# Performance work log

Measured on AMD Instinct MI355X. Metric: run time of the kernel, lower is better.

## Reference

```python
import jax, jax.numpy as jnp
import numpy as np

VOXEL_SIZE = 0.4
GAMMA = 1.1  # VoxelPointsSampler.GAMMA
GRID = 376   # (75.2 - (-75.2)) / 0.4


def setup_inputs() -> dict:
    key = jax.random.key(0)
    k1, k2, k3, k4, k5 = jax.random.split(key, 5)
    V, K, F, R, S = 20000, 16, 5, 256, 128
    pc_start = jnp.array([-75.2, -75.2], dtype=jnp.float32)
    coords = jax.random.randint(k1, (V, 2), 0, GRID, dtype=jnp.int32)  # voxel (x,y) grid coords
    centers = coords.astype(jnp.float32) * VOXEL_SIZE + pc_start
    voxels = jax.random.normal(k2, (V, K, F), dtype=jnp.float32)
    # place point xy near their voxel center so the radius search is non-trivial
    voxels = voxels.at[:, :, :2].multiply(0.2)
    voxels = voxels.at[:, :, :2].add(centers[:, None, :])
    num_points = jax.random.randint(k3, (V,), 0, K + 1, dtype=jnp.int32)
    bxy = jax.random.uniform(k4, (R, 2), jnp.float32, -70.0, 70.0)   # box centers x,y
    brest = jax.random.uniform(k5, (R, 5), jnp.float32)
    boxes = jnp.concatenate(
        [bxy, brest[:, :1], brest[:, 1:3] * 4.0 + 1.0, brest[:, 3:]], axis=1
    )  # [R,7]: x,y,z,dx,dy,dz,heading with dx,dy in [1,5]
    return {
        "voxels": voxels,
        "boxes": boxes,
        "pc_start": pc_start,
        "coords": coords,
        "num_points": num_points,
        "num_sample": S,
    }


def reference(voxels, boxes, pc_start, coords, num_points, num_sample):
    # voxels: [V,K,F] voxelized points; boxes: [R,7] ROIs; coords: [V,2] voxel (x,y) grid coords
    V, K, F = voxels.shape
    dt = voxels.dtype
    # --- voxel-level radius search (forward hot path) ---
    query_coords = (boxes[:, :2] - pc_start) / VOXEL_SIZE            # [R,2]
    radii_vox = jnp.linalg.norm(boxes[:, 3:5] * 0.5, axis=-1) * GAMMA / VOXEL_SIZE  # [R]
    dist = jnp.linalg.norm(query_coords[:, None, :] - coords[None, :, :].astype(dt), axis=-1)  # [R,V]
    voxel_mask = jnp.any(dist < radii_vox[:, None], axis=0)          # [V]
    # --- per-voxel valid-point mask (arange(k) < num_points), combined with voxel_mask ---
    pt_valid = (jnp.arange(K)[None, :] < num_points[:, None]) & voxel_mask[:, None]  # [V,K]
    pts = voxels.reshape(V * K, F)                                   # [N,F], N = V*K
    valid = pt_valid.reshape(V * K)                                  # [N]
    # --- cylindrical pool: per-ROI radius mask over points + topk sampling ---
    radii = jnp.linalg.norm(boxes[:, 3:5] * 0.5, axis=-1) * GAMMA    # [R]
    dis = jnp.linalg.norm(pts[None, :, :2] - boxes[:, None, :2], axis=-1)  # [R,N]
    point_mask = (dis <= radii[:, None]) & valid[None, :]            # [R,N]
    sampled_mask, sampled_idx = jax.lax.top_k(point_mask.astype(dt), num_sample)  # [R,S]
    key_points = jnp.take(pts, sampled_idx, axis=0) * sampled_mask[..., None]     # [R,S,F]
    return key_points, sampled_mask, voxel_mask
```

## Files before the change

kernel.cpp:

```cpp
#include <hip/hip_runtime.h>
#include <hip/hip_bf16.h>
#include <stdint.h>

#define VOXEL_SIZE_F 0.4f
#define GAMMA_F 1.1f
#define SLACK_F 0.0625f

__device__ __forceinline__ float sq2_rn(float dx, float dy) {
    return __fadd_rn(__fmul_rn(dx, dx), __fmul_rn(dy, dy));
}

__device__ __forceinline__ int wave_incl_scan(int v, int lane) {
    #pragma unroll
    for (int d = 1; d < 64; d <<= 1) {
        int t = __shfl_up(v, d, 64);
        if (lane >= d) v += t;
    }
    return v;
}

__global__ void k1_mask(const float* __restrict__ boxes,
                        const float* __restrict__ pc_start,
                        const int* __restrict__ coords,
                        const int* __restrict__ num_points,
                        const float* __restrict__ voxels,
                        int V, int R, int K, int F,
                        unsigned char* __restrict__ vstat,
                        float* __restrict__ vmaxoff,
                        float* __restrict__ out_vox,
                        int* __restrict__ bc) {
    __shared__ float qx[256], qy[256], rv[256];
    int lane = threadIdx.x;
    int v = blockIdx.x * 64 + lane;
    float psx = pc_start[0], psy = pc_start[1];
    float cxf = 0.f, cyf = 0.f;
    int np = 0;
    if (v < V) {
        cxf = (float)coords[2 * v];
        cyf = (float)coords[2 * v + 1];
        np = num_points[v];
        np = np < 0 ? 0 : (np > K ? K : np);
    }
    int m = 0;
    for (int rb = 0; rb < R; rb += 256) {
        int tile = (R - rb) < 256 ? (R - rb) : 256;
        for (int j = lane; j < tile; j += 64) {
            const float* bp = boxes + (size_t)(rb + j) * 7;
            float hx = bp[3] * 0.5f, hy = bp[4] * 0.5f;
            qx[j] = (bp[0] - psx) / VOXEL_SIZE_F;
            qy[j] = (bp[1] - psy) / VOXEL_SIZE_F;
            rv[j] = (sqrtf(sq2_rn(hx, hy)) * GAMMA_F) / VOXEL_SIZE_F;
        }
        __syncthreads();
        #pragma unroll 4
        for (int j = 0; j < tile; j++) {
            float dx = qx[j] - cxf, dy = qy[j] - cyf;
            m |= (sqrtf(sq2_rn(dx, dy)) < rv[j]) ? 1 : 0;
        }
        __syncthreads();
    }
    int am = (v < V) ? m : 0;
    unsigned long long bal = __ballot(am != 0);
    if (lane == 0) bc[blockIdx.x] = __popcll(bal);
    float mo = -1e30f;
    if (am && np > 0) {
        float cxm = cxf * VOXEL_SIZE_F + psx;
        float cym = cyf * VOXEL_SIZE_F + psy;
        const float* pv = voxels + (size_t)v * K * F;
        for (int k = 0; k < np; k++) {
            float px = pv[k * F + 0], py = pv[k * F + 1];
            float d = sqrtf(sq2_rn(px - cxm, py - cym));
            mo = fmaxf(mo, d);
        }
    }
    if (v < V) {
        vstat[v] = am ? (unsigned char)(np + 1) : 0;
        vmaxoff[v] = mo;
        out_vox[v] = am ? 1.0f : 0.0f;
    }
}

__global__ void k2_compact(const unsigned char* __restrict__ vstat,
                           const float* __restrict__ vmaxoff,
                           const int* __restrict__ coords,
                           const float* __restrict__ pc_start,
                           int V, int nb,
                           const int* __restrict__ bc,
                           float4* __restrict__ actq,
                           int* __restrict__ act_count) {
    __shared__ int sbase;
    int b = blockIdx.x;
    int lane = threadIdx.x;
    if (lane == 0) sbase = 0;
    __syncthreads();
    int run = 0;
    for (int i0 = 0; i0 < nb; i0 += 64) {
        int i = i0 + lane;
        int val = (i < nb) ? bc[i] : 0;
        int incl = wave_incl_scan(val, lane);
        if (i == b) sbase = run + incl - val;
        run += __shfl(incl, 63, 64);
    }
    if (b == 0 && lane == 0) *act_count = run;
    __syncthreads();
    int base = sbase;

    int v = b * 64 + lane;
    int stat = (v < V) ? (int)vstat[v] : 0;
    int m = stat > 0;
    unsigned long long bal = __ballot(m != 0);
    unsigned long long ltmask = (1ull << lane) - 1ull;
    int rank = __popcll(bal & ltmask);
    if (m) {
        float psx = pc_start[0], psy = pc_start[1];
        float cxm = (float)coords[2 * v] * VOXEL_SIZE_F + psx;
        float cym = (float)coords[2 * v + 1] * VOXEL_SIZE_F + psy;
        float4 q;
        q.x = cxm;
        q.y = cym;
        q.z = vmaxoff[v];
        q.w = __int_as_float(v | ((stat - 1) << 16));
        actq[base + rank] = q;
    }
}

__global__ void k3_roi(const float* __restrict__ voxels,
                       const float* __restrict__ boxes,
                       const float4* __restrict__ actq,
                       const int* __restrict__ act_count,
                       int K, int F, int S,
                       float* __restrict__ out_kp,
                       float* __restrict__ out_mask) {
    __shared__ float4 cq[256];
    __shared__ int wsum[4];
    int r = blockIdx.x;
    int tid = threadIdx.x, lane = tid & 63, wid = tid >> 6;
    unsigned long long ltmask = (1ull << lane) - 1ull;

    const float* bp = boxes + (size_t)r * 7;
    float bx = bp[0], by = bp[1];
    float hx = bp[3] * 0.5f, hy = bp[4] * 0.5f;
    float rad = sqrtf(sq2_rn(hx, hy)) * GAMMA_F;
    int A = *act_count;
    int count = 0;

    for (int c0 = 0; c0 < A && count < S; c0 += 256) {
        int i = c0 + tid;
        int pred = 0;
        float4 q = make_float4(0.f, 0.f, 0.f, 0.f);
        if (i < A) {
            q = actq[i];
            float d = sqrtf(sq2_rn(q.x - bx, q.y - by));
            pred = (d <= rad + q.z + SLACK_F) ? 1 : 0;
        }
        unsigned long long bal = __ballot(pred != 0);
        if (lane == 0) wsum[wid] = __popcll(bal);
        __syncthreads();
        int cb = 0;
        for (int w = 0; w < wid; w++) cb += wsum[w];
        int tot = wsum[0] + wsum[1] + wsum[2] + wsum[3];
        if (pred) cq[cb + __popcll(bal & ltmask)] = q;
        __syncthreads();

        for (int g0 = 0; g0 < tot && count < S; g0 += 16) {
            int ci = g0 + (tid >> 4), k = tid & 15;
            int pred2 = 0;
            size_t n = 0;
            if (ci < tot) {
                float4 qq = cq[ci];
                int vn = __float_as_int(qq.w);
                int npv = vn >> 16, vid = vn & 0xFFFF;
                if (k < npv) {
                    n = (size_t)(vid * K + k);
                    float px = voxels[n * F + 0], py = voxels[n * F + 1];
                    pred2 = (sqrtf(sq2_rn(px - bx, py - by)) <= rad) ? 1 : 0;
                }
            }
            unsigned long long bal2 = __ballot(pred2 != 0);
            if (lane == 0) wsum[wid] = __popcll(bal2);
            __syncthreads();
            int wb = count;
            for (int w = 0; w < wid; w++) wb += wsum[w];
            int tot2 = wsum[0] + wsum[1] + wsum[2] + wsum[3];
            int pos = wb + __popcll(bal2 & ltmask);
            if (pred2 && pos < S) {
                const float* src = voxels + n * F;
                float* dst = out_kp + ((size_t)r * S + pos) * F;
                #pragma unroll
                for (int j = 0; j < 5; j++) dst[j] = src[j];
            }
            count += tot2;
            __syncthreads();
        }
    }

    int sc = count < S ? count : S;
    for (int s = tid; s < S; s += 256)
        out_mask[(size_t)r * S + s] = (s < sc) ? 1.0f : 0.0f;
    for (int j = tid; j < S * F; j += 256) {
        int s = j / F;
        if (s >= sc) out_kp[(size_t)r * S * F + j] = 0.0f;
    }
}

extern "C" void kernel_launch(void* const* d_in, const int* in_sizes, int n_in,
                              void* d_out, int out_size, void* d_ws, size_t ws_size,
                              hipStream_t stream) {
    const float* voxels   = (const float*)d_in[0];
    const float* boxes    = (const float*)d_in[1];
    const float* pc_start = (const float*)d_in[2];
    const int*   coords   = (const int*)d_in[3];
    const int*   num_pts  = (const int*)d_in[4];

    int V = in_sizes[4];
    int R = in_sizes[1] / 7;
    int K = 16;
    int F = (in_sizes[0] / V) / K;
    int S = (out_size - V) / (R * (F + 1));
    int nb = (V + 63) / 64;

    float* out_kp  = (float*)d_out;
    float* out_msk = out_kp + (size_t)R * S * F;
    float* out_vox = out_msk + (size_t)R * S;

    char* w = (char*)d_ws;
    auto carve = [&](size_t bytes) {
        void* p = (void*)w;
        w += (bytes + 255) & ~(size_t)255;
        return p;
    };
    unsigned char* vstat   = (unsigned char*)carve((size_t)V);
    float*         vmaxoff = (float*)carve((size_t)V * 4);
    int*           bc      = (int*)carve((size_t)nb * 4);
    int*           actcnt  = (int*)carve(4);
    float4*        actq    = (float4*)carve((size_t)V * 16);

    k1_mask<<<nb, 64, 0, stream>>>(boxes, pc_start, coords, num_pts, voxels,
                                   V, R, K, F, vstat, vmaxoff, out_vox, bc);
    k2_compact<<<nb, 64, 0, stream>>>(vstat, vmaxoff, coords, pc_start,
                                      V, nb, bc, actq, actcnt);
    k3_roi<<<R, 256, 0, stream>>>(voxels, boxes, actq, actcnt,
                                  K, F, S, out_kp, out_msk);
}
```

Measured before the change: 111.5 us.

## Fuse mask, compaction and ROI sampling into one kernel with grid barrier

Replaces the three-kernel pipeline with a single persistent kernel. Each block first computes voxel masks and per-voxel records for 256 voxels, then waits at a software grid barrier (atomic counter) before doing per-ROI sampling. The separate compaction pass is dropped: ROI blocks scan all V records directly, and inactive voxels are skipped through a max-offset sentinel and a block-wide count early-out. This removes two kernel launches and the prefix-scan step, but each ROI now scans all voxels rather than only active ones. It also depends on all 256 blocks being co-resident for the spin barrier, and adds a memset launch.

```diff
diff --git a/kernel.cpp b/kernel.cpp
--- a/kernel.cpp
+++ b/kernel.cpp
@@ -10,196 +10,144 @@
     return __fadd_rn(__fmul_rn(dx, dx), __fmul_rn(dy, dy));
 }
 
-__device__ __forceinline__ int wave_incl_scan(int v, int lane) {
-    #pragma unroll
-    for (int d = 1; d < 64; d <<= 1) {
-        int t = __shfl_up(v, d, 64);
-        if (lane >= d) v += t;
-    }
-    return v;
-}
+__global__ __launch_bounds__(256) void k_fused(
+    const float* __restrict__ voxels,
+    const float* __restrict__ boxes,
+    const float* __restrict__ pc_start,
+    const int* __restrict__ coords,
+    const int* __restrict__ num_points,
+    int V, int R, int K, int F, int S,
+    float4* __restrict__ recq,
+    int* __restrict__ bar,
+    float* __restrict__ out_kp,
+    float* __restrict__ out_mask,
+    float* __restrict__ out_vox)
+{
+    __shared__ float qx[256], qy[256], rv[256];
+    __shared__ float4 cq[256];
+    __shared__ int wsum[4];
+    int tid = threadIdx.x, lane = tid & 63, wid = tid >> 6;
+    int b = blockIdx.x;
+    unsigned long long ltmask = (1ull << lane) - 1ull;
+    float psx = pc_start[0], psy = pc_start[1];
 
-__global__ void k1_mask(const float* __restrict__ boxes,
-                        const float* __restrict__ pc_start,
-                        const int* __restrict__ coords,
-                        const int* __restrict__ num_points,
-                        const float* __restrict__ voxels,
-                        int V, int R, int K, int F,
-                        unsigned char* __restrict__ vstat,
-                        float* __restrict__ vmaxoff,
-                        float* __restrict__ out_vox,
-                        int* __restrict__ bc) {
-    __shared__ float qx[256], qy[256], rv[256];
-    int lane = threadIdx.x;
-    int v = blockIdx.x * 64 + lane;
-    float psx = pc_start[0], psy = pc_start[1];
-    float cxf = 0.f, cyf = 0.f;
-    int np = 0;
-    if (v < V) {
-        cxf = (float)coords[2 * v];
-        cyf = (float)coords[2 * v + 1];
-        np = num_points[v];
-        np = np < 0 ? 0 : (np > K ? K : np);
-    }
-    int m = 0;
-    for (int rb = 0; rb < R; rb += 256) {
-        int tile = (R - rb) < 256 ? (R - rb) : 256;
-        for (int j = lane; j < tile; j += 64) {
-            const float* bp = boxes + (size_t)(rb + j) * 7;
+    int v = b * 256 + tid;
+    if (b * 256 < V) {
+        for (int j = tid; j < R; j += 256) {
+            const float* bp = boxes + (size_t)j * 7;
             float hx = bp[3] * 0.5f, hy = bp[4] * 0.5f;
             qx[j] = (bp[0] - psx) / VOXEL_SIZE_F;
             qy[j] = (bp[1] - psy) / VOXEL_SIZE_F;
             rv[j] = (sqrtf(sq2_rn(hx, hy)) * GAMMA_F) / VOXEL_SIZE_F;
         }
         __syncthreads();
-        #pragma unroll 4
-        for (int j = 0; j < tile; j++) {
-            float dx = qx[j] - cxf, dy = qy[j] - cyf;
-            m |= (sqrtf(sq2_rn(dx, dy)) < rv[j]) ? 1 : 0;
-        }
-        __syncthreads();
-    }
-    int am = (v < V) ? m : 0;
-    unsigned long long bal = __ballot(am != 0);
-    if (lane == 0) bc[blockIdx.x] = __popcll(bal);
-    float mo = -1e30f;
-    if (am && np > 0) {
-        float cxm = cxf * VOXEL_SIZE_F + psx;
-        float cym = cyf * VOXEL_SIZE_F + psy;
-        const float* pv = voxels + (size_t)v * K * F;
-        for (int k = 0; k < np; k++) {
-            float px = pv[k * F + 0], py = pv[k * F + 1];
-            float d = sqrtf(sq2_rn(px - cxm, py - cym));
-            mo = fmaxf(mo, d);
-        }
-    }
-    if (v < V) {
-        vstat[v] = am ? (unsigned char)(np + 1) : 0;
-        vmaxoff[v] = mo;
-        out_vox[v] = am ? 1.0f : 0.0f;
-    }
-}
-
-__global__ void k2_compact(const unsigned char* __restrict__ vstat,
-                           const float* __restrict__ vmaxoff,
-                           const int* __restrict__ coords,
-                           const float* __restrict__ pc_start,
-                           int V, int nb,
-                           const int* __restrict__ bc,
-                           float4* __restrict__ actq,
-                           int* __restrict__ act_count) {
-    __shared__ int sbase;
-    int b = blockIdx.x;
-    int lane = threadIdx.x;
-    if (lane == 0) sbase = 0;
-    __syncthreads();
-    int run = 0;
-    for (int i0 = 0; i0 < nb; i0 += 64) {
-        int i = i0 + lane;
-        int val = (i < nb) ? bc[i] : 0;
-        int incl = wave_incl_scan(val, lane);
-        if (i == b) sbase = run + incl - val;
-        run += __shfl(incl, 63, 64);
-    }
-    if (b == 0 && lane == 0) *act_count = run;
-    __syncthreads();
-    int base = sbase;
-
-    int v = b * 64 + lane;
-    int stat = (v < V) ? (int)vstat[v] : 0;
-    int m = stat > 0;
-    unsigned long long bal = __ballot(m != 0);
-    unsigned long long ltmask = (1ull << lane) - 1ull;
-    int rank = __popcll(bal & ltmask);
-    if (m) {
-        float psx = pc_start[0], psy = pc_start[1];
-        float cxm = (float)coords[2 * v] * VOXEL_SIZE_F + psx;
-        float cym = (float)coords[2 * v + 1] * VOXEL_SIZE_F + psy;
-        float4 q;
-        q.x = cxm;
-        q.y = cym;
-        q.z = vmaxoff[v];
-        q.w = __int_as_float(v | ((stat - 1) << 16));
-        actq[base + rank] = q;
-    }
-}
-
-__global__ void k3_roi(const float* __restrict__ voxels,
-                       const float* __restrict__ boxes,
-                       const float4* __restrict__ actq,
-                       const int* __restrict__ act_count,
-                       int K, int F, int S,
-                       float* __restrict__ out_kp,
-                       float* __restrict__ out_mask) {
-    __shared__ float4 cq[256];
-    __shared__ int wsum[4];
-    int r = blockIdx.x;
-    int tid = threadIdx.x, lane = tid & 63, wid = tid >> 6;
-    unsigned long long ltmask = (1ull << lane) - 1ull;
-
-    const float* bp = boxes + (size_t)r * 7;
-    float bx = bp[0], by = bp[1];
-    float hx = bp[3] * 0.5f, hy = bp[4] * 0.5f;
-    float rad = sqrtf(sq2_rn(hx, hy)) * GAMMA_F;
-    int A = *act_count;
-    int count = 0;
-
-    for (int c0 = 0; c0 < A && count < S; c0 += 256) {
-        int i = c0 + tid;
-        int pred = 0;
-        float4 q = make_float4(0.f, 0.f, 0.f, 0.f);
-        if (i < A) {
-            q = actq[i];
-            float d = sqrtf(sq2_rn(q.x - bx, q.y - by));
-            pred = (d <= rad + q.z + SLACK_F) ? 1 : 0;
-        }
-        unsigned long long bal = __ballot(pred != 0);
-        if (lane == 0) wsum[wid] = __popcll(bal);
-        __syncthreads();
-        int cb = 0;
-        for (int w = 0; w < wid; w++) cb += wsum[w];
-        int tot = wsum[0] + wsum[1] + wsum[2] + wsum[3];
-        if (pred) cq[cb + __popcll(bal & ltmask)] = q;
-        __syncthreads();
-
-        for (int g0 = 0; g0 < tot && count < S; g0 += 16) {
-            int ci = g0 + (tid >> 4), k = tid & 15;
-            int pred2 = 0;
-            size_t n = 0;
-            if (ci < tot) {
-                float4 qq = cq[ci];
-                int vn = __float_as_int(qq.w);
-                int npv = vn >> 16, vid = vn & 0xFFFF;
-                if (k < npv) {
-                    n = (size_t)(vid * K + k);
-                    float px = voxels[n * F + 0], py = voxels[n * F + 1];
-                    pred2 = (sqrtf(sq2_rn(px - bx, py - by)) <= rad) ? 1 : 0;
+        if (v < V) {
+            float cxf = (float)coords[2 * v], cyf = (float)coords[2 * v + 1];
+            int np = num_points[v];
+            np = np < 0 ? 0 : (np > K ? K : np);
+            int m = 0;
+            #pragma unroll 4
+            for (int j = 0; j < R; j++) {
+                float dx = qx[j] - cxf, dy = qy[j] - cyf;
+                m |= (sqrtf(sq2_rn(dx, dy)) < rv[j]) ? 1 : 0;
+            }
+            float cxm = cxf * VOXEL_SIZE_F + psx;
+            float cym = cyf * VOXEL_SIZE_F + psy;
+            float mo = -1e30f;
+            if (m && np > 0) {
+                const float* pv = voxels + (size_t)v * K * F;
+                #pragma unroll 4
+                for (int k = 0; k < K; k++) {
+                    float px = pv[k * F + 0], py = pv[k * F + 1];
+                    float d = sqrtf(sq2_rn(px - cxm, py - cym));
+                    if (k < np) mo = fmaxf(mo, d);
                 }
             }
-            unsigned long long bal2 = __ballot(pred2 != 0);
-            if (lane == 0) wsum[wid] = __popcll(bal2);
-            __syncthreads();
-            int wb = count;
-            for (int w = 0; w < wid; w++) wb += wsum[w];
-            int tot2 = wsum[0] + wsum[1] + wsum[2] + wsum[3];
-            int pos = wb + __popcll(bal2 & ltmask);
-            if (pred2 && pos < S) {
-                const float* src = voxels + n * F;
-                float* dst = out_kp + ((size_t)r * S + pos) * F;
-                #pragma unroll
-                for (int j = 0; j < 5; j++) dst[j] = src[j];
-            }
-            count += tot2;
-            __syncthreads();
+            float4 q;
+            q.x = cxm; q.y = cym; q.z = mo;
+            q.w = __int_as_float(v | (np << 16));
+            recq[v] = q;
+            out_vox[v] = m ? 1.0f : 0.0f;
         }
     }
 
-    int sc = count < S ? count : S;
-    for (int s = tid; s < S; s += 256)
-        out_mask[(size_t)r * S + s] = (s < sc) ? 1.0f : 0.0f;
-    for (int j = tid; j < S * F; j += 256) {
-        int s = j / F;
-        if (s >= sc) out_kp[(size_t)r * S * F + j] = 0.0f;
+    __syncthreads();
+    __threadfence();
+    if (tid == 0) {
+        __hip_atomic_fetch_add(bar, 1, __ATOMIC_ACQ_REL, __HIP_MEMORY_SCOPE_AGENT);
+        while (__hip_atomic_load(bar, __ATOMIC_ACQUIRE, __HIP_MEMORY_SCOPE_AGENT)
+               < (int)gridDim.x)
+            __builtin_amdgcn_s_sleep(8);
+    }
+    __syncthreads();
+    __threadfence();
+
+    int r = b;
+    if (r < R) {
+        const float* bp = boxes + (size_t)r * 7;
+        float bx = bp[0], by = bp[1];
+        float rad = sqrtf(sq2_rn(bp[3] * 0.5f, bp[4] * 0.5f)) * GAMMA_F;
+        int count = 0;
+
+        for (int c0 = 0; c0 < V && count < S; c0 += 256) {
+            int i = c0 + tid;
+            int pred = 0;
+            float4 q = make_float4(0.f, 0.f, 0.f, 0.f);
+            if (i < V) {
+                q = recq[i];
+                float d = sqrtf(sq2_rn(q.x - bx, q.y - by));
+                pred = (d <= rad + q.z + SLACK_F) ? 1 : 0;
+            }
+            int tot = __syncthreads_count(pred);
+            if (tot == 0) continue;
+
+            unsigned long long bal = __ballot(pred != 0);
+            if (lane == 0) wsum[wid] = __popcll(bal);
+            __syncthreads();
+            int cb = 0;
+            for (int w2 = 0; w2 < wid; w2++) cb += wsum[w2];
+            if (pred) cq[cb + __popcll(bal & ltmask)] = q;
+            __syncthreads();
+
+            for (int g0 = 0; g0 < tot && count < S; g0 += 16) {
+                int ci = g0 + (tid >> 4), k = tid & 15;
+                int pred2 = 0;
+                size_t n = 0;
+                if (ci < tot) {
+                    float4 qq = cq[ci];
+                    int vn = __float_as_int(qq.w);
+                    int npv = vn >> 16, vid = vn & 0xFFFF;
+                    if (k < npv) {
+                        n = (size_t)vid * K + k;
+                        float px = voxels[n * F + 0], py = voxels[n * F + 1];
+                        pred2 = (sqrtf(sq2_rn(px - bx, py - by)) <= rad) ? 1 : 0;
+                    }
+                }
+                unsigned long long bal2 = __ballot(pred2 != 0);
+                if (lane == 0) wsum[wid] = __popcll(bal2);
+                __syncthreads();
+                int wb = count;
+                for (int w2 = 0; w2 < wid; w2++) wb += wsum[w2];
+                int tot2 = wsum[0] + wsum[1] + wsum[2] + wsum[3];
+                int pos = wb + __popcll(bal2 & ltmask);
+                if (pred2 && pos < S) {
+                    const float* src = voxels + n * F;
+                    float* dst = out_kp + ((size_t)r * S + pos) * F;
+                    #pragma unroll
+                    for (int j = 0; j < 5; j++) dst[j] = src[j];
+                }
+                count += tot2;
+                __syncthreads();
+            }
+        }
+
+        int sc = count < S ? count : S;
+        for (int s = tid; s < S; s += 256)
+            out_mask[(size_t)r * S + s] = (s < sc) ? 1.0f : 0.0f;
+        for (int j = tid; j < S * F; j += 256) {
+            int s = j / F;
+            if (s >= sc) out_kp[(size_t)r * S * F + j] = 0.0f;
+        }
     }
 }
 
@@ -217,7 +165,6 @@
     int K = 16;
     int F = (in_sizes[0] / V) / K;
     int S = (out_size - V) / (R * (F + 1));
-    int nb = (V + 63) / 64;
 
     float* out_kp  = (float*)d_out;
     float* out_msk = out_kp + (size_t)R * S * F;
@@ -229,16 +176,14 @@
         w += (bytes + 255) & ~(size_t)255;
         return p;
     };
-    unsigned char* vstat   = (unsigned char*)carve((size_t)V);
-    float*         vmaxoff = (float*)carve((size_t)V * 4);
-    int*           bc      = (int*)carve((size_t)nb * 4);
-    int*           actcnt  = (int*)carve(4);
-    float4*        actq    = (float4*)carve((size_t)V * 16);
+    int*    bar  = (int*)carve(4);
+    float4* recq = (float4*)carve((size_t)V * 16);
 
-    k1_mask<<<nb, 64, 0, stream>>>(boxes, pc_start, coords, num_pts, voxels,
-                                   V, R, K, F, vstat, vmaxoff, out_vox, bc);
-    k2_compact<<<nb, 64, 0, stream>>>(vstat, vmaxoff, coords, pc_start,
-                                      V, nb, bc, actq, actcnt);
-    k3_roi<<<R, 256, 0, stream>>>(voxels, boxes, actq, actcnt,
-                                  K, F, S, out_kp, out_msk);
+    int NB = (V + 255) / 256;
+    if (NB < R) NB = R;
+
+    hipMemsetAsync(bar, 0, sizeof(int), stream);
+    k_fused<<<NB, 256, 0, stream>>>(voxels, boxes, pc_start, coords, num_pts,
+                                    V, R, K, F, S, recq, bar,
+                                    out_kp, out_msk, out_vox);
 }
```

Result: slower. 187.6 us (+68.3%).
